# Optimization experiments

Hardware: AMD Instinct MI355X
Metric: run time of the kernel (lower is better)

The kernel has to match this reference:

```python
import jax, jax.numpy as jnp
import numpy as np

N_RES = 320
C_Z = 128
NUM_HEAD = 4
HEAD_DIM = C_Z // NUM_HEAD  # 32
LN_EPS = 1e-5


def layer_norm(x, scale, offset):
    mean = jnp.mean(x, axis=-1, keepdims=True)
    var = jnp.var(x, axis=-1, keepdims=True)
    return (x - mean) * jax.lax.rsqrt(var + LN_EPS) * scale + offset


def setup_inputs() -> dict:
    key = jax.random.key(0)
    ks = jax.random.split(key, 12)
    d = {
        'pair_act': jax.random.normal(ks[0], (N_RES, N_RES, C_Z), jnp.float32),
        'affine_act': jax.random.normal(ks[1], (N_RES, N_RES, C_Z), jnp.float32),
        'pair_mask': jnp.ones((N_RES, N_RES), jnp.float32),
        'pair_ln_scale': jnp.ones((C_Z,), jnp.float32),
        'pair_ln_offset': jnp.zeros((C_Z,), jnp.float32),
        'affine_ln_scale': jnp.ones((C_Z,), jnp.float32),
        'affine_ln_offset': jnp.zeros((C_Z,), jnp.float32),
        'feat_2d_weights': jax.random.normal(ks[2], (C_Z, NUM_HEAD), jnp.float32) / 0.8796256610342398,
        'query_w': jax.random.normal(ks[3], (C_Z, NUM_HEAD, HEAD_DIM), jnp.float32) * 0.05,
        'key_w': jax.random.normal(ks[4], (C_Z, NUM_HEAD, HEAD_DIM), jnp.float32) * 0.05,
        'value_w': jax.random.normal(ks[5], (C_Z, NUM_HEAD, HEAD_DIM), jnp.float32) * 0.05,
        'gating_w': jax.random.normal(ks[6], (C_Z, NUM_HEAD, HEAD_DIM), jnp.float32) * 0.05,
        'output_w': jax.random.normal(ks[7], (NUM_HEAD, HEAD_DIM, C_Z), jnp.float32) * 0.05,
    }
    return d


def reference(pair_act, affine_act, pair_mask,
              pair_ln_scale, pair_ln_offset, affine_ln_scale, affine_ln_offset,
              feat_2d_weights, query_w, key_w, value_w, gating_w, output_w):
    # orientation == 'per_row' -> no swapaxes
    pair_ln = layer_norm(pair_act, pair_ln_scale, pair_ln_offset)          # [N,N,c]
    affine_ln = layer_norm(affine_act, affine_ln_scale, affine_ln_offset)  # [N,N,c]

    # padding bias [N,1,1,N]
    bias = (1e9 * (pair_mask - 1.0))[:, None, None, :]
    # nonbatched pair bias [H,N,N]
    nonbatched_bias = jnp.einsum('qkc,ch->hqk', affine_ln, feat_2d_weights)

    # attention (q_data == m_data == pair_ln)
    scale = HEAD_DIM ** (-0.5)
    q = jnp.einsum('bqa,ahc->bqhc', pair_ln, query_w) * scale
    k = jnp.einsum('bka,ahc->bkhc', pair_ln, key_w)
    v = jnp.einsum('bka,ahc->bkhc', pair_ln, value_w)

    logits = jnp.einsum('bqhc,bkhc->bhqk', q, k) + bias + nonbatched_bias[None]
    weights = jax.nn.softmax(logits, axis=-1)
    weighted_avg = jnp.einsum('bhqk,bkhc->bqhc', weights, v)

    gate = jax.nn.sigmoid(jnp.einsum('bqc,chv->bqhv', pair_ln, gating_w))
    weighted_avg = weighted_avg * gate

    out = jnp.einsum('bqhc,hco->bqo', weighted_avg, output_w)  # [N,N,c_z]
    return out
```

## Files before the change

kernel.cpp:

```cpp
#include <hip/hip_runtime.h>
#include <hip/hip_bf16.h>

#define N_RES 320
#define C_Z   128
#define NH    4
#define HD    32
#define M_TOT (N_RES*N_RES)
#define LN_EPS 1e-5f
#define QSCALE 0.17677669529663687f
#define LOG2E  1.4426950408889634f

typedef __attribute__((ext_vector_type(8))) short short8;
typedef __attribute__((ext_vector_type(4))) float floatx4;
typedef __attribute__((ext_vector_type(4))) unsigned uintx4;

#define OFF_MASK 0
#define OFF_PLS  102400
#define OFF_PLO  102528
#define OFF_ALS  102656
#define OFF_ALO  102784
#define OFF_FWT  102912
#define OFF_WQT  104960
#define OFF_WKT  121344
#define OFF_WVT  137728
#define OFF_WGT  154112
#define OFF_WOT  170496
#define ARENA_N  186880

__device__ __forceinline__ float u16_to_f(unsigned short s){
    union { unsigned u; float f; } v; v.u = ((unsigned)s) << 16; return v.f;
}
__device__ __forceinline__ unsigned short bf16r(float f){
    union { __hip_bfloat16 b; unsigned short s; } v; v.b = __float2bfloat16(f); return v.s;
}
__device__ __forceinline__ unsigned pack2(float a, float b){
    return (unsigned)bf16r(a) | ((unsigned)bf16r(b) << 16);
}
__device__ __forceinline__ float ld_dual(const void* s, size_t i, bool isbf){
    return isbf ? u16_to_f(((const unsigned short*)s)[i]) : ((const float*)s)[i];
}

__device__ __forceinline__ short8 xpose_frag(unsigned A0, unsigned A1,
                                             unsigned B0, unsigned B1, int lane)
{
#if __has_builtin(__builtin_amdgcn_permlane32_swap) && __has_builtin(__builtin_amdgcn_permlane16_swap)
    (void)lane;
    auto uv0 = __builtin_amdgcn_permlane32_swap(A0, B0, false, false);
    auto uv1 = __builtin_amdgcn_permlane32_swap(A1, B1, false, false);
    auto t02 = __builtin_amdgcn_permlane16_swap(uv0[0], uv0[1], false, false);
    auto t13 = __builtin_amdgcn_permlane16_swap(uv1[0], uv1[1], false, false);
    uintx4 u = { t02[0], t13[0], t02[1], t13[1] };
#else
    bool hi32 = lane >= 32, oddq = (lane & 16) != 0;
    unsigned A0x = __shfl_xor(A0, 32, 64), B0x = __shfl_xor(B0, 32, 64);
    unsigned A1x = __shfl_xor(A1, 32, 64), B1x = __shfl_xor(B1, 32, 64);
    unsigned U0 = hi32 ? B0x : A0, V0 = hi32 ? B0 : A0x;
    unsigned U1 = hi32 ? B1x : A1, V1 = hi32 ? B1 : A1x;
    unsigned U0x = __shfl_xor(U0, 16, 64), V0x = __shfl_xor(V0, 16, 64);
    unsigned U1x = __shfl_xor(U1, 16, 64), V1x = __shfl_xor(V1, 16, 64);
    unsigned T0 = oddq ? V0x : U0, T2 = oddq ? V0 : U0x;
    unsigned T1 = oddq ? V1x : U1, T3 = oddq ? V1 : U1x;
    uintx4 u = { T0, T1, T2, T3 };
#endif
    union { uintx4 u; short8 s; } cvt; cvt.u = u;
    return cvt.s;
}

__global__ __launch_bounds__(256) void k_conv_all(
    const void* __restrict__ s_mask, const void* __restrict__ s_pls,
    const void* __restrict__ s_plo,  const void* __restrict__ s_als,
    const void* __restrict__ s_alo,  const void* __restrict__ s_fw,
    const void* __restrict__ s_wq,   const void* __restrict__ s_wk,
    const void* __restrict__ s_wv,   const void* __restrict__ s_wg,
    const void* __restrict__ s_wo,
    unsigned short* __restrict__ arena, const unsigned* __restrict__ probe)
{
    int gid = blockIdx.x * 256 + threadIdx.x;
    bool isbf = (probe[0] & 0xffffu) != 0;
    float val;
    if (gid < OFF_PLS)      val = ld_dual(s_mask, gid, isbf);
    else if (gid < OFF_PLO) val = ld_dual(s_pls, gid - OFF_PLS, isbf);
    else if (gid < OFF_ALS) val = ld_dual(s_plo, gid - OFF_PLO, isbf);
    else if (gid < OFF_ALO) val = ld_dual(s_als, gid - OFF_ALS, isbf);
    else if (gid < OFF_FWT) val = ld_dual(s_alo, gid - OFF_ALO, isbf);
    else if (gid < OFF_WQT){
        int local = gid - OFF_FWT, hh = local >> 7, c = local & 127;
        val = (hh < 4) ? ld_dual(s_fw, c*NH + hh, isbf) : 0.0f;
    } else if (gid < OFF_WOT){
        int seg = (gid - OFF_WQT) >> 14;
        int local = (gid - OFF_WQT) & 16383;
        int hc = local >> 7, z = local & 127;
        const void* src = (seg == 0) ? s_wq : (seg == 1) ? s_wk : (seg == 2) ? s_wv : s_wg;
        val = ld_dual(src, z*128 + hc, isbf);
    } else {
        int local = gid - OFF_WOT, o = local >> 7, hc = local & 127;
        val = ld_dual(s_wo, hc*128 + o, isbf);
    }
    arena[gid] = bf16r(val);
}

__global__ __launch_bounds__(256) void k_ln_fused(
    const void* __restrict__ pair, const void* __restrict__ affine,
    const unsigned short* __restrict__ pls, const unsigned short* __restrict__ plo,
    const unsigned short* __restrict__ als, const unsigned short* __restrict__ alo,
    const unsigned short* __restrict__ fwpT,
    unsigned short* __restrict__ pl, float* __restrict__ nb,
    const unsigned* __restrict__ probe)
{
    int bid = blockIdx.x;
    bool isPair = bid < 1600;
    int tid = threadIdx.x, lane = tid & 63, wave = tid >> 6;
    int c16 = lane & 15, quad = lane >> 4, rb = quad * 4;
    int m0 = (isPair ? bid : bid - 1600) * 64 + wave * 16;
    bool isbf = (probe[0] & 0xffffu) != 0;

    const void* src = isPair ? pair : affine;
    const unsigned short* sc = isPair ? pls : als;
    const unsigned short* of = isPair ? plo : alo;

    float x[32];
    if (isbf){
        const short8* a8 = (const short8*)src;
        #pragma unroll
        for (int ks = 0; ks < 4; ++ks){
            short8 t = a8[(size_t)(m0 + c16)*16 + ks*4 + quad];
            #pragma unroll
            for (int j = 0; j < 8; ++j) x[ks*8+j] = u16_to_f((unsigned short)t[j]);
        }
    } else {
        const floatx4* a4 = (const floatx4*)src;
        #pragma unroll
        for (int ks = 0; ks < 4; ++ks){
            floatx4 f0 = a4[(size_t)(m0 + c16)*32 + ks*8 + quad*2];
            floatx4 f1 = a4[(size_t)(m0 + c16)*32 + ks*8 + quad*2 + 1];
            #pragma unroll
            for (int j = 0; j < 4; ++j){ x[ks*8+j] = f0[j]; x[ks*8+4+j] = f1[j]; }
        }
    }
    float s = 0.f, ss = 0.f;
    #pragma unroll
    for (int j = 0; j < 32; ++j){ s += x[j]; ss += x[j]*x[j]; }
    s  += __shfl_xor(s, 16, 64);  s  += __shfl_xor(s, 32, 64);
    ss += __shfl_xor(ss, 16, 64); ss += __shfl_xor(ss, 32, 64);
    float mean = s * (1.0f/128.0f);
    float var  = ss * (1.0f/128.0f) - mean*mean;
    float rs   = rsqrtf(var + LN_EPS);

    const short8* sc8 = (const short8*)sc;
    const short8* of8 = (const short8*)of;

    if (isPair){
        short8* pl8 = (short8*)pl;
        #pragma unroll
        for (int ks = 0; ks < 4; ++ks){
            short8 scv = sc8[ks*4 + quad], ofv = of8[ks*4 + quad];
            short8 lf;
            #pragma unroll
            for (int j = 0; j < 8; ++j){
                float l = (x[ks*8+j] - mean) * rs * u16_to_f((unsigned short)scv[j])
                        + u16_to_f((unsigned short)ofv[j]);
                lf[j] = (short)bf16r(l);
            }
            pl8[(size_t)(m0 + c16)*16 + ks*4 + quad] = lf;
        }
    } else {
        short8 lf[4], lg[4];
        #pragma unroll
        for (int ks = 0; ks < 4; ++ks){
            short8 scv = sc8[ks*4 + quad], ofv = of8[ks*4 + quad];
            #pragma unroll
            for (int j = 0; j < 8; ++j){
                float l = (x[ks*8+j] - mean) * rs * u16_to_f((unsigned short)scv[j])
                        + u16_to_f((unsigned short)ofv[j]);
                unsigned short hi = bf16r(l);
                lf[ks][j] = (short)hi;
                lg[ks][j] = (short)bf16r(l - u16_to_f(hi));
            }
        }
        floatx4 acc = {0.f, 0.f, 0.f, 0.f};
        const short8* fw8 = (const short8*)fwpT;
        #pragma unroll
        for (int ks = 0; ks < 4; ++ks){
            short8 fwf = fw8[c16*16 + ks*4 + quad];
            acc = __builtin_amdgcn_mfma_f32_16x16x32_bf16(lf[ks], fwf, acc, 0, 0, 0);
            acc = __builtin_amdgcn_mfma_f32_16x16x32_bf16(lg[ks], fwf, acc, 0, 0, 0);
        }
        acc = acc * LOG2E;
        if (c16 < 4)
            *(floatx4*)&nb[(size_t)c16 * M_TOT + m0 + rb] = acc;
    }
}

__global__ __launch_bounds__(256) void k_nbmax(float* __restrict__ nb)
{
    int tid = threadIdx.x, lane = tid & 63, wave = tid >> 6;
    int row = blockIdx.x * 4 + wave;
    float* r = nb + (size_t)row * N_RES;
    floatx4 v = *(const floatx4*)&r[lane*4];
    float x5 = r[256 + lane];
    float m = fmaxf(fmaxf(v[0], v[1]), fmaxf(v[2], v[3]));
    m = fmaxf(m, x5);
    #pragma unroll
    for (int d = 32; d; d >>= 1) m = fmaxf(m, __shfl_xor(m, d, 64));
    float M = m + 8.0f;
    floatx4 vo = { v[0]-M, v[1]-M, v[2]-M, v[3]-M };
    *(floatx4*)&r[lane*4] = vo;
    r[256 + lane] = x5 - M;
}

__global__ __launch_bounds__(640, 4) void k_attn(
    const unsigned short* __restrict__ pl,
    const unsigned short* __restrict__ wqT, const unsigned short* __restrict__ wkT,
    const unsigned short* __restrict__ wvT, const unsigned short* __restrict__ wgT,
    const unsigned short* __restrict__ maskc, const float* __restrict__ nb,
    unsigned short* __restrict__ wab)
{
    __shared__ __align__(16) unsigned short Ks[320*40];
    __shared__ __align__(16) unsigned short Vt[32*328];
    __shared__ __align__(16) float biasl[320];

    int b = blockIdx.x, h = blockIdx.y;
    int tid = threadIdx.x, lane = tid & 63, wave = tid >> 6;
    int c16 = lane & 15, quad = lane >> 4, rb = quad * 4;

    const short8* plrow8 = (const short8*)(pl + (size_t)b * N_RES * C_Z);
    const short8* Ks8 = (const short8*)Ks;
    const short8* Vt8 = (const short8*)Vt;
    const short8* wqT8 = (const short8*)wqT;
    const short8* wkT8 = (const short8*)wkT;
    const short8* wvT8 = (const short8*)wvT;
    const short8* wgT8 = (const short8*)wgT;
    floatx4 Z = {0.f, 0.f, 0.f, 0.f};

    if (tid < 320)
        biasl[tid] = (LOG2E * 1e9f) * (u16_to_f(maskc[(size_t)b * N_RES + tid]) - 1.0f);

    #pragma unroll 1
    for (int mt = wave; mt < 20; mt += 10){
        short8 a[4];
        #pragma unroll
        for (int ks = 0; ks < 4; ++ks)
            a[ks] = plrow8[(mt*16 + c16)*16 + ks*4 + quad];

        #pragma unroll
        for (int ct = 0; ct < 2; ++ct){
            int hc = h*HD + ct*16 + c16;
            floatx4 acc = Z;
            #pragma unroll
            for (int ks = 0; ks < 4; ++ks){
                short8 bw = wkT8[hc*16 + ks*4 + quad];
                acc = __builtin_amdgcn_mfma_f32_16x16x32_bf16(a[ks], bw, acc, 0, 0, 0);
            }
            #pragma unroll
            for (int i = 0; i < 4; ++i)
                Ks[(mt*16 + rb + i)*40 + ct*16 + c16] = bf16r(acc[i]);
        }
        #pragma unroll
        for (int ct = 0; ct < 2; ++ct){
            int hc = h*HD + ct*16 + c16;
            floatx4 acc = Z;
            #pragma unroll
            for (int ks = 0; ks < 4; ++ks){
                short8 bw = wvT8[hc*16 + ks*4 + quad];
                acc = __builtin_amdgcn_mfma_f32_16x16x32_bf16(bw, a[ks], acc, 0, 0, 0);
            }
            #pragma unroll
            for (int i = 0; i < 4; ++i)
                Vt[(ct*16 + rb + i)*328 + mt*16 + c16] = bf16r(acc[i]);
        }
    }
    __syncthreads();

    {
        int m0A = wave * 16, m0B = (wave + 10) * 16;

        short8 qfA, qfB;
        {
            floatx4 qa0 = Z, qa1 = Z, qb0 = Z, qb1 = Z;
            #pragma unroll
            for (int ks = 0; ks < 4; ++ks){
                short8 plA = plrow8[(m0A + c16)*16 + ks*4 + quad];
                short8 plB = plrow8[(m0B + c16)*16 + ks*4 + quad];
                short8 w0 = wqT8[(h*HD + c16)*16 + ks*4 + quad];
                short8 w1 = wqT8[(h*HD + 16 + c16)*16 + ks*4 + quad];
                qa0 = __builtin_amdgcn_mfma_f32_16x16x32_bf16(w0, plA, qa0, 0, 0, 0);
                qa1 = __builtin_amdgcn_mfma_f32_16x16x32_bf16(w1, plA, qa1, 0, 0, 0);
                qb0 = __builtin_amdgcn_mfma_f32_16x16x32_bf16(w0, plB, qb0, 0, 0, 0);
                qb1 = __builtin_amdgcn_mfma_f32_16x16x32_bf16(w1, plB, qb1, 0, 0, 0);
            }
            const float QS = QSCALE * LOG2E;
            qfA = xpose_frag(pack2(qa0[0]*QS, qa0[1]*QS), pack2(qa0[2]*QS, qa0[3]*QS),
                             pack2(qa1[0]*QS, qa1[1]*QS), pack2(qa1[2]*QS, qa1[3]*QS), lane);
            qfB = xpose_frag(pack2(qb0[0]*QS, qb0[1]*QS), pack2(qb0[2]*QS, qb0[3]*QS),
                             pack2(qb1[0]*QS, qb1[1]*QS), pack2(qb1[2]*QS, qb1[3]*QS), lane);
        }

        float lA = 0.f, lB = 0.f;
        floatx4 a0A = Z, a1A = Z, a0B = Z, a1B = Z;
        const float* nbqA = nb + (size_t)h * M_TOT + (size_t)(m0A + c16) * N_RES;
        const float* nbqB = nb + (size_t)h * M_TOT + (size_t)(m0B + c16) * N_RES;

        #pragma unroll 1
        for (int kt2 = 0; kt2 < 10; ++kt2){
            int k0 = kt2 * 32;
            short8 kfa = Ks8[(k0 + c16)*5 + quad];
            short8 kfb = Ks8[(k0 + 16 + c16)*5 + quad];
            floatx4 saA = __builtin_amdgcn_mfma_f32_16x16x32_bf16(kfa, qfA, Z, 0, 0, 0);
            floatx4 sbA = __builtin_amdgcn_mfma_f32_16x16x32_bf16(kfb, qfA, Z, 0, 0, 0);
            floatx4 saB = __builtin_amdgcn_mfma_f32_16x16x32_bf16(kfa, qfB, Z, 0, 0, 0);
            floatx4 sbB = __builtin_amdgcn_mfma_f32_16x16x32_bf16(kfb, qfB, Z, 0, 0, 0);
            floatx4 bia = *(const floatx4*)&biasl[k0 + rb];
            floatx4 bib = *(const floatx4*)&biasl[k0 + 16 + rb];
            floatx4 nbaA = *(const floatx4*)&nbqA[k0 + rb];
            floatx4 nbbA = *(const floatx4*)&nbqA[k0 + 16 + rb];
            floatx4 nbaB = *(const floatx4*)&nbqB[k0 + rb];
            floatx4 nbbB = *(const floatx4*)&nbqB[k0 + 16 + rb];
            float paA[4], pbA[4], paB[4], pbB[4], tsA = 0.f, tsB = 0.f;
            #pragma unroll
            for (int i = 0; i < 4; ++i){
                paA[i] = exp2f(saA[i] + nbaA[i] + bia[i]);
                pbA[i] = exp2f(sbA[i] + nbbA[i] + bib[i]);
                paB[i] = exp2f(saB[i] + nbaB[i] + bia[i]);
                pbB[i] = exp2f(sbB[i] + nbbB[i] + bib[i]);
                tsA += paA[i] + pbA[i];
                tsB += paB[i] + pbB[i];
            }
            lA += tsA;  lB += tsB;
            short8 ptA = xpose_frag(pack2(paA[0], paA[1]), pack2(paA[2], paA[3]),
                                    pack2(pbA[0], pbA[1]), pack2(pbA[2], pbA[3]), lane);
            short8 ptB = xpose_frag(pack2(paB[0], paB[1]), pack2(paB[2], paB[3]),
                                    pack2(pbB[0], pbB[1]), pack2(pbB[2], pbB[3]), lane);
            short8 v0 = Vt8[c16*41 + kt2*4 + quad];
            short8 v1 = Vt8[(16 + c16)*41 + kt2*4 + quad];
            a0A = __builtin_amdgcn_mfma_f32_16x16x32_bf16(v0, ptA, a0A, 0, 0, 0);
            a1A = __builtin_amdgcn_mfma_f32_16x16x32_bf16(v1, ptA, a1A, 0, 0, 0);
            a0B = __builtin_amdgcn_mfma_f32_16x16x32_bf16(v0, ptB, a0B, 0, 0, 0);
            a1B = __builtin_amdgcn_mfma_f32_16x16x32_bf16(v1, ptB, a1B, 0, 0, 0);
        }

        lA += __shfl_xor(lA, 16, 64);  lA += __shfl_xor(lA, 32, 64);
        lB += __shfl_xor(lB, 16, 64);  lB += __shfl_xor(lB, 32, 64);
        float invA = 1.0f / lA, invB = 1.0f / lB;

        floatx4 g0A = Z, g1A = Z, g0B = Z, g1B = Z;
        #pragma unroll
        for (int ks = 0; ks < 4; ++ks){
            short8 plA = plrow8[(m0A + c16)*16 + ks*4 + quad];
            short8 plB = plrow8[(m0B + c16)*16 + ks*4 + quad];
            short8 u0 = wgT8[(h*HD + c16)*16 + ks*4 + quad];
            short8 u1 = wgT8[(h*HD + 16 + c16)*16 + ks*4 + quad];
            g0A = __builtin_amdgcn_mfma_f32_16x16x32_bf16(u0, plA, g0A, 0, 0, 0);
            g1A = __builtin_amdgcn_mfma_f32_16x16x32_bf16(u1, plA, g1A, 0, 0, 0);
            g0B = __builtin_amdgcn_mfma_f32_16x16x32_bf16(u0, plB, g0B, 0, 0, 0);
            g1B = __builtin_amdgcn_mfma_f32_16x16x32_bf16(u1, plB, g1B, 0, 0, 0);
        }
        float oA[8], oB[8];
        #pragma unroll
        for (int i = 0; i < 4; ++i){
            oA[i]     = a0A[i] * invA * (1.0f/(1.0f + __expf(-g0A[i])));
            oA[4 + i] = a1A[i] * invA * (1.0f/(1.0f + __expf(-g1A[i])));
            oB[i]     = a0B[i] * invB * (1.0f/(1.0f + __expf(-g0B[i])));
            oB[4 + i] = a1B[i] * invB * (1.0f/(1.0f + __expf(-g1B[i])));
        }
        size_t baseA = (size_t)h * (M_TOT*HD) + (size_t)(b*N_RES + m0A + c16) * HD;
        size_t baseB = (size_t)h * (M_TOT*HD) + (size_t)(b*N_RES + m0B + c16) * HD;
        uint2 sA0 = { pack2(oA[0], oA[1]), pack2(oA[2], oA[3]) };
        uint2 sA1 = { pack2(oA[4], oA[5]), pack2(oA[6], oA[7]) };
        uint2 sB0 = { pack2(oB[0], oB[1]), pack2(oB[2], oB[3]) };
        uint2 sB1 = { pack2(oB[4], oB[5]), pack2(oB[6], oB[7]) };
        *(uint2*)&wab[baseA + rb]      = sA0;
        *(uint2*)&wab[baseA + 16 + rb] = sA1;
        *(uint2*)&wab[baseB + rb]      = sB0;
        *(uint2*)&wab[baseB + 16 + rb] = sB1;
    }
}

__global__ __launch_bounds__(256, 4) void k_outproj(
    const unsigned short* __restrict__ wab, const unsigned short* __restrict__ woT,
    void* __restrict__ out, const unsigned* __restrict__ probe)
{
    int tid = threadIdx.x, lane = tid & 63, wave = tid >> 6;
    int c16 = lane & 15, quad = lane >> 4, rb = quad * 4;
    int m0 = blockIdx.x * 64 + wave * 16;
    bool isbf = (probe[0] & 0xffffu) != 0;

    const short8* wab8 = (const short8*)wab;
    const short8* woT8 = (const short8*)woT;
    floatx4 Z = {0.f, 0.f, 0.f, 0.f};

    short8 a[4];
    #pragma unroll
    for (int ks = 0; ks < 4; ++ks)
        a[ks] = wab8[(size_t)ks * (M_TOT*4) + (size_t)(m0 + c16)*4 + quad];

    #pragma unroll 1
    for (int nt = 0; nt < 8; ++nt){
        floatx4 acc = Z;
        #pragma unroll
        for (int ks = 0; ks < 4; ++ks){
            short8 bf = woT8[(nt*16 + c16)*16 + ks*4 + quad];
            acc = __builtin_amdgcn_mfma_f32_16x16x32_bf16(a[ks], bf, acc, 0, 0, 0);
        }
        #pragma unroll
        for (int i = 0; i < 4; ++i){
            size_t idx = (size_t)(m0 + rb + i)*C_Z + nt*16 + c16;
            if (isbf) ((unsigned short*)out)[idx] = bf16r(acc[i]);
            else      ((float*)out)[idx] = acc[i];
        }
    }
}

extern "C" void kernel_launch(void* const* d_in, const int* in_sizes, int n_in,
                              void* d_out, int out_size, void* d_ws, size_t ws_size,
                              hipStream_t stream)
{
    const unsigned* probe = (const unsigned*)d_in[3];

    char* w = (char*)d_ws;
    unsigned short* arena = (unsigned short*)w;
    unsigned short* mask_c = arena + OFF_MASK;
    unsigned short* pls_c  = arena + OFF_PLS;
    unsigned short* plo_c  = arena + OFF_PLO;
    unsigned short* als_c  = arena + OFF_ALS;
    unsigned short* alo_c  = arena + OFF_ALO;
    unsigned short* fwT_c  = arena + OFF_FWT;
    unsigned short* wqT_c  = arena + OFF_WQT;
    unsigned short* wkT_c  = arena + OFF_WKT;
    unsigned short* wvT_c  = arena + OFF_WVT;
    unsigned short* wgT_c  = arena + OFF_WGT;
    unsigned short* woT_c  = arena + OFF_WOT;
    float*          nb     = (float*)(w + 524288);
    unsigned short* pl     = (unsigned short*)(w + 2162688);
    unsigned short* wab    = (unsigned short*)(w + 28377088);

    k_conv_all<<<730, 256, 0, stream>>>(d_in[2], d_in[3], d_in[4], d_in[5], d_in[6],
                                        d_in[7], d_in[8], d_in[9], d_in[10], d_in[11],
                                        d_in[12], arena, probe);
    k_ln_fused<<<3200, 256, 0, stream>>>(d_in[0], d_in[1], pls_c, plo_c, als_c, alo_c,
                                         fwT_c, pl, nb, probe);
    k_nbmax   <<<320, 256, 0, stream>>>(nb);
    k_attn    <<<dim3(N_RES, NH), 640, 0, stream>>>(pl, wqT_c, wkT_c, wvT_c, wgT_c,
                                                    mask_c, nb, wab);
    k_outproj <<<1600, 256, 0, stream>>>(wab, woT_c, d_out, probe);
}
```

Before: 348.0 us.

## Merge weight conversion into layernorm kernel and unroll attention loops

The separate weight-conversion kernel is folded into the layernorm kernel as extra blocks, removing one launch. The layernorm path now reads scale, offset and feat_2d weights directly from the raw inputs instead of waiting on the converted arena. The two attention loops change from unroll 1 to unroll 2, and the gate sigmoid switches from __expf to exp2f. The tradeoffs are more per-element global loads with a format branch inside the layernorm path, and higher register pressure in the attention kernel from the unrolling.

```diff
diff --git a/kernel.cpp b/kernel.cpp
--- a/kernel.cpp
+++ b/kernel.cpp
@@ -66,57 +66,55 @@
     return cvt.s;
 }
 
-__global__ __launch_bounds__(256) void k_conv_all(
+__global__ __launch_bounds__(256) void k_lnconv(
+    const void* __restrict__ pair, const void* __restrict__ affine,
     const void* __restrict__ s_mask, const void* __restrict__ s_pls,
     const void* __restrict__ s_plo,  const void* __restrict__ s_als,
     const void* __restrict__ s_alo,  const void* __restrict__ s_fw,
     const void* __restrict__ s_wq,   const void* __restrict__ s_wk,
     const void* __restrict__ s_wv,   const void* __restrict__ s_wg,
     const void* __restrict__ s_wo,
-    unsigned short* __restrict__ arena, const unsigned* __restrict__ probe)
-{
-    int gid = blockIdx.x * 256 + threadIdx.x;
-    bool isbf = (probe[0] & 0xffffu) != 0;
-    float val;
-    if (gid < OFF_PLS)      val = ld_dual(s_mask, gid, isbf);
-    else if (gid < OFF_PLO) val = ld_dual(s_pls, gid - OFF_PLS, isbf);
-    else if (gid < OFF_ALS) val = ld_dual(s_plo, gid - OFF_PLO, isbf);
-    else if (gid < OFF_ALO) val = ld_dual(s_als, gid - OFF_ALS, isbf);
-    else if (gid < OFF_FWT) val = ld_dual(s_alo, gid - OFF_ALO, isbf);
-    else if (gid < OFF_WQT){
-        int local = gid - OFF_FWT, hh = local >> 7, c = local & 127;
-        val = (hh < 4) ? ld_dual(s_fw, c*NH + hh, isbf) : 0.0f;
-    } else if (gid < OFF_WOT){
-        int seg = (gid - OFF_WQT) >> 14;
-        int local = (gid - OFF_WQT) & 16383;
-        int hc = local >> 7, z = local & 127;
-        const void* src = (seg == 0) ? s_wq : (seg == 1) ? s_wk : (seg == 2) ? s_wv : s_wg;
-        val = ld_dual(src, z*128 + hc, isbf);
-    } else {
-        int local = gid - OFF_WOT, o = local >> 7, hc = local & 127;
-        val = ld_dual(s_wo, hc*128 + o, isbf);
-    }
-    arena[gid] = bf16r(val);
-}
-
-__global__ __launch_bounds__(256) void k_ln_fused(
-    const void* __restrict__ pair, const void* __restrict__ affine,
-    const unsigned short* __restrict__ pls, const unsigned short* __restrict__ plo,
-    const unsigned short* __restrict__ als, const unsigned short* __restrict__ alo,
-    const unsigned short* __restrict__ fwpT,
+    unsigned short* __restrict__ arena,
     unsigned short* __restrict__ pl, float* __restrict__ nb,
     const unsigned* __restrict__ probe)
 {
     int bid = blockIdx.x;
+    int tid = threadIdx.x;
+    bool isbf = (probe[0] & 0xffffu) != 0;
+
+    if (bid >= 3200){
+        int gid = (bid - 3200) * 256 + tid;
+        float val;
+        if (gid < OFF_PLS)      val = ld_dual(s_mask, gid, isbf);
+        else if (gid < OFF_PLO) val = ld_dual(s_pls, gid - OFF_PLS, isbf);
+        else if (gid < OFF_ALS) val = ld_dual(s_plo, gid - OFF_PLO, isbf);
+        else if (gid < OFF_ALO) val = ld_dual(s_als, gid - OFF_ALS, isbf);
+        else if (gid < OFF_FWT) val = ld_dual(s_alo, gid - OFF_ALO, isbf);
+        else if (gid < OFF_WQT){
+            int local = gid - OFF_FWT, hh = local >> 7, c = local & 127;
+            val = (hh < 4) ? ld_dual(s_fw, c*NH + hh, isbf) : 0.0f;
+        } else if (gid < OFF_WOT){
+            int seg = (gid - OFF_WQT) >> 14;
+            int local = (gid - OFF_WQT) & 16383;
+            int hc = local >> 7, z = local & 127;
+            const void* src = (seg == 0) ? s_wq : (seg == 1) ? s_wk : (seg == 2) ? s_wv : s_wg;
+            val = ld_dual(src, z*128 + hc, isbf);
+        } else {
+            int local = gid - OFF_WOT, o = local >> 7, hc = local & 127;
+            val = ld_dual(s_wo, hc*128 + o, isbf);
+        }
+        arena[gid] = bf16r(val);
+        return;
+    }
+
     bool isPair = bid < 1600;
-    int tid = threadIdx.x, lane = tid & 63, wave = tid >> 6;
+    int lane = tid & 63, wave = tid >> 6;
     int c16 = lane & 15, quad = lane >> 4, rb = quad * 4;
     int m0 = (isPair ? bid : bid - 1600) * 64 + wave * 16;
-    bool isbf = (probe[0] & 0xffffu) != 0;
 
     const void* src = isPair ? pair : affine;
-    const unsigned short* sc = isPair ? pls : als;
-    const unsigned short* of = isPair ? plo : alo;
+    const void* sc  = isPair ? s_pls : s_als;
+    const void* of  = isPair ? s_plo : s_alo;
 
     float x[32];
     if (isbf){
@@ -146,19 +144,16 @@
     float var  = ss * (1.0f/128.0f) - mean*mean;
     float rs   = rsqrtf(var + LN_EPS);
 
-    const short8* sc8 = (const short8*)sc;
-    const short8* of8 = (const short8*)of;
-
     if (isPair){
         short8* pl8 = (short8*)pl;
         #pragma unroll
         for (int ks = 0; ks < 4; ++ks){
-            short8 scv = sc8[ks*4 + quad], ofv = of8[ks*4 + quad];
             short8 lf;
             #pragma unroll
             for (int j = 0; j < 8; ++j){
-                float l = (x[ks*8+j] - mean) * rs * u16_to_f((unsigned short)scv[j])
-                        + u16_to_f((unsigned short)ofv[j]);
+                int c = ks*32 + quad*8 + j;
+                float l = (x[ks*8+j] - mean) * rs * ld_dual(sc, c, isbf)
+                        + ld_dual(of, c, isbf);
                 lf[j] = (short)bf16r(l);
             }
             pl8[(size_t)(m0 + c16)*16 + ks*4 + quad] = lf;
@@ -167,21 +162,26 @@
         short8 lf[4], lg[4];
         #pragma unroll
         for (int ks = 0; ks < 4; ++ks){
-            short8 scv = sc8[ks*4 + quad], ofv = of8[ks*4 + quad];
             #pragma unroll
             for (int j = 0; j < 8; ++j){
-                float l = (x[ks*8+j] - mean) * rs * u16_to_f((unsigned short)scv[j])
-                        + u16_to_f((unsigned short)ofv[j]);
+                int c = ks*32 + quad*8 + j;
+                float l = (x[ks*8+j] - mean) * rs * ld_dual(sc, c, isbf)
+                        + ld_dual(of, c, isbf);
                 unsigned short hi = bf16r(l);
                 lf[ks][j] = (short)hi;
                 lg[ks][j] = (short)bf16r(l - u16_to_f(hi));
             }
         }
         floatx4 acc = {0.f, 0.f, 0.f, 0.f};
-        const short8* fw8 = (const short8*)fwpT;
-        #pragma unroll
-        for (int ks = 0; ks < 4; ++ks){
-            short8 fwf = fw8[c16*16 + ks*4 + quad];
+        #pragma unroll
+        for (int ks = 0; ks < 4; ++ks){
+            short8 fwf;
+            #pragma unroll
+            for (int j = 0; j < 8; ++j){
+                int c = ks*32 + quad*8 + j;
+                fwf[j] = (c16 < 4) ? (short)bf16r(ld_dual(s_fw, (size_t)c*NH + c16, isbf))
+                                   : (short)0;
+            }
             acc = __builtin_amdgcn_mfma_f32_16x16x32_bf16(lf[ks], fwf, acc, 0, 0, 0);
             acc = __builtin_amdgcn_mfma_f32_16x16x32_bf16(lg[ks], fwf, acc, 0, 0, 0);
         }
@@ -235,7 +235,7 @@
     if (tid < 320)
         biasl[tid] = (LOG2E * 1e9f) * (u16_to_f(maskc[(size_t)b * N_RES + tid]) - 1.0f);
 
-    #pragma unroll 1
+    #pragma unroll 2
     for (int mt = wave; mt < 20; mt += 10){
         short8 a[4];
         #pragma unroll
@@ -300,7 +300,7 @@
         const float* nbqA = nb + (size_t)h * M_TOT + (size_t)(m0A + c16) * N_RES;
         const float* nbqB = nb + (size_t)h * M_TOT + (size_t)(m0B + c16) * N_RES;
 
-        #pragma unroll 1
+        #pragma unroll 2
         for (int kt2 = 0; kt2 < 10; ++kt2){
             int k0 = kt2 * 32;
             short8 kfa = Ks8[(k0 + c16)*5 + quad];
@@ -357,10 +357,10 @@
         float oA[8], oB[8];
         #pragma unroll
         for (int i = 0; i < 4; ++i){
-            oA[i]     = a0A[i] * invA * (1.0f/(1.0f + __expf(-g0A[i])));
-            oA[4 + i] = a1A[i] * invA * (1.0f/(1.0f + __expf(-g1A[i])));
-            oB[i]     = a0B[i] * invB * (1.0f/(1.0f + __expf(-g0B[i])));
-            oB[4 + i] = a1B[i] * invB * (1.0f/(1.0f + __expf(-g1B[i])));
+            oA[i]     = a0A[i] * invA * (1.0f/(1.0f + exp2f(-LOG2E*g0A[i])));
+            oA[4 + i] = a1A[i] * invA * (1.0f/(1.0f + exp2f(-LOG2E*g1A[i])));
+            oB[i]     = a0B[i] * invB * (1.0f/(1.0f + exp2f(-LOG2E*g0B[i])));
+            oB[4 + i] = a1B[i] * invB * (1.0f/(1.0f + exp2f(-LOG2E*g1B[i])));
         }
         size_t baseA = (size_t)h * (M_TOT*HD) + (size_t)(b*N_RES + m0A + c16) * HD;
         size_t baseB = (size_t)h * (M_TOT*HD) + (size_t)(b*N_RES + m0B + c16) * HD;
@@ -419,11 +419,6 @@
     char* w = (char*)d_ws;
     unsigned short* arena = (unsigned short*)w;
     unsigned short* mask_c = arena + OFF_MASK;
-    unsigned short* pls_c  = arena + OFF_PLS;
-    unsigned short* plo_c  = arena + OFF_PLO;
-    unsigned short* als_c  = arena + OFF_ALS;
-    unsigned short* alo_c  = arena + OFF_ALO;
-    unsigned short* fwT_c  = arena + OFF_FWT;
     unsigned short* wqT_c  = arena + OFF_WQT;
     unsigned short* wkT_c  = arena + OFF_WKT;
     unsigned short* wvT_c  = arena + OFF_WVT;
@@ -433,13 +428,12 @@
     unsigned short* pl     = (unsigned short*)(w + 2162688);
     unsigned short* wab    = (unsigned short*)(w + 28377088);
 
-    k_conv_all<<<730, 256, 0, stream>>>(d_in[2], d_in[3], d_in[4], d_in[5], d_in[6],
-                                        d_in[7], d_in[8], d_in[9], d_in[10], d_in[11],
-                                        d_in[12], arena, probe);
-    k_ln_fused<<<3200, 256, 0, stream>>>(d_in[0], d_in[1], pls_c, plo_c, als_c, alo_c,
-                                         fwT_c, pl, nb, probe);
-    k_nbmax   <<<320, 256, 0, stream>>>(nb);
-    k_attn    <<<dim3(N_RES, NH), 640, 0, stream>>>(pl, wqT_c, wkT_c, wvT_c, wgT_c,
-                                                    mask_c, nb, wab);
-    k_outproj <<<1600, 256, 0, stream>>>(wab, woT_c, d_out, probe);
-}
+    k_lnconv<<<3930, 256, 0, stream>>>(d_in[0], d_in[1], d_in[2], d_in[3], d_in[4],
+                                       d_in[5], d_in[6], d_in[7], d_in[8], d_in[9],
+                                       d_in[10], d_in[11], d_in[12],
+                                       arena, pl, nb, probe);
+    k_nbmax  <<<320, 256, 0, stream>>>(nb);
+    k_attn   <<<dim3(N_RES, NH), 640, 0, stream>>>(pl, wqT_c, wkT_c, wvT_c, wgT_c,
+                                                   mask_c, nb, wab);
+    k_outproj<<<1600, 256, 0, stream>>>(wab, woT_c, d_out, probe);
+}
```

Result: no change. 353.2 us (+1.5%).
